# Kernel tuning notes

Hardware: AMD Instinct MI355X
Metric: run time of the kernel (lower is better)

Reference implementation:

```python
import jax, jax.numpy as jnp
import numpy as np

N_NODES = 50000
N_EDGES = 800000
N_GRAPHS = 512


def gcn_conv(x, W, b, src, dst, n_nodes):
    # Standard PyG GCNConv: linear transform, add self-loops, D^-1/2 (A+I) D^-1/2 aggregation.
    x = x @ W  # [N, out]
    loop = jnp.arange(n_nodes, dtype=src.dtype)
    s = jnp.concatenate([src, loop])  # [E+N]
    d = jnp.concatenate([dst, loop])
    deg = jax.ops.segment_sum(jnp.ones_like(d, dtype=x.dtype), d, num_segments=n_nodes)
    dinv = jnp.where(deg > 0, jax.lax.rsqrt(jnp.maximum(deg, 1e-12)), 0.0)
    norm = dinv[s] * dinv[d]  # [E+N]
    msg = x[s] * norm[:, None]  # gather + scale
    out = jax.ops.segment_sum(msg, d, num_segments=n_nodes)  # scatter-add
    return out + b


def setup_inputs() -> dict:
    key = jax.random.key(0)
    ks = jax.random.split(key, 10)
    x = jax.random.normal(ks[0], (N_NODES, 128), dtype=jnp.float32)
    edge_index = jax.random.randint(ks[1], (2, N_EDGES), 0, N_NODES, dtype=jnp.int64)
    batch = jnp.sort(jax.random.randint(ks[2], (N_NODES,), 0, N_GRAPHS, dtype=jnp.int64))
    y = jax.random.randint(ks[3], (N_GRAPHS,), 0, 4, dtype=jnp.int64)
    W1 = jax.random.normal(ks[4], (128, 64), dtype=jnp.float32) * (1.0 / np.sqrt(128))
    b1 = jnp.zeros((64,), dtype=jnp.float32)
    W2 = jax.random.normal(ks[5], (64, 64), dtype=jnp.float32) * (1.0 / np.sqrt(64))
    b2 = jnp.zeros((64,), dtype=jnp.float32)
    Wfc = jax.random.normal(ks[6], (64, 4), dtype=jnp.float32) * (1.0 / np.sqrt(64))
    bfc = jnp.zeros((4,), dtype=jnp.float32)
    return {"x": x, "edge_index": edge_index, "batch": batch, "y": y,
            "W1": W1, "b1": b1, "W2": W2, "b2": b2, "Wfc": Wfc, "bfc": bfc}


def reference(x, edge_index, batch, y, W1, b1, W2, b2, Wfc, bfc):
    src, dst = edge_index[0], edge_index[1]
    h = jax.nn.relu(gcn_conv(x, W1, b1, src, dst, N_NODES))
    h = jax.nn.relu(gcn_conv(h, W2, b2, src, dst, N_NODES))
    # global mean pool over graph ids
    sums = jax.ops.segment_sum(h, batch, num_segments=N_GRAPHS)  # [G, out]
    cnts = jax.ops.segment_sum(jnp.ones((h.shape[0],), h.dtype), batch, num_segments=N_GRAPHS)
    pooled = sums / jnp.maximum(cnts, 1.0)[:, None]
    logits = pooled @ Wfc + bfc
    logp = jax.nn.log_softmax(logits, axis=1)
    return (logp, y)
```

## Files before the change

kernel.cpp:

```cpp
#include <hip/hip_runtime.h>
#include <hip/hip_fp16.h>
#include <math.h>

#define N_NODES 50000
#define N_EDGES 800000
#define N_GRAPHS 512
#define NBKT 196
#define SENT N_NODES
#define EPB 2048
#define NSEG 391
#define CAP_C 48
#define NBLK_B2 392
#define CAP_SH 8192
#define NBLK_GM 782
#define PREP_GRID (NBLK_B2 + NBLK_GM)
#define N_GROUPS 6272
#define NBLK_G 1568

typedef float v2f __attribute__((ext_vector_type(2)));
typedef float f32x4 __attribute__((ext_vector_type(4)));
typedef short s16x8 __attribute__((ext_vector_type(8)));

#define OFF_DINV    0u
#define OFF_GGRP    200704u
#define OFF_CNTM    250880u
#define OFF_TMP     557568u
#define OFF_SORTED  15271680u
#define OFF_XS8_1   28116736u
#define OFF_XS8_2   31316992u
#define OFF_H2      34517248u

__device__ __forceinline__ unsigned short f2bf(float f) {
    unsigned int u = __float_as_uint(f);
    u += 0x7FFFu + ((u >> 16) & 1u);
    return (unsigned short)(u >> 16);
}

__global__ __launch_bounds__(256) void binA(const int* __restrict__ src, const int* __restrict__ dst,
                                            int* __restrict__ cntmat, unsigned int* __restrict__ tmp,
                                            unsigned int* __restrict__ x1, unsigned int* __restrict__ x2,
                                            float* __restrict__ dinv) {
    __shared__ int cnt[256];
    int t = threadIdx.x;
    cnt[t] = 0;
    if (blockIdx.x == 0) {
        if (t < 16) x1[N_NODES * 16 + t] = 0;
        else if (t < 32) x2[N_NODES * 16 + (t - 16)] = 0;
        else if (t >= 64 && t < 240) dinv[N_NODES + (t - 64)] = 0.0f;
    }
    __syncthreads();
    int e0 = blockIdx.x * EPB;
#pragma unroll
    for (int i = 0; i < 8; ++i) {
        int e = e0 + i * 256 + t;
        if (e < N_EDGES) {
            int s = src[e], d = dst[e];
            int b = d >> 8;
            int p = atomicAdd(&cnt[b], 1);
            tmp[(b * NSEG + blockIdx.x) * CAP_C + p] =
                (unsigned int)s | ((unsigned int)(d & 255) << 17);
        }
    }
    __syncthreads();
    if (t < NBKT) cntmat[blockIdx.x * NBKT + t] = cnt[t];
}

__global__ __launch_bounds__(256) void prep(const unsigned int* __restrict__ tmp,
                                            const int* __restrict__ cntmat,
                                            int* __restrict__ sorted, int2* __restrict__ ggrp,
                                            float* __restrict__ dinv,
                                            const float* __restrict__ X, const float* __restrict__ W1,
                                            unsigned int* __restrict__ xs8) {
    __shared__ __align__(16) char pool[35072];
    int t = threadIdx.x;

    if (blockIdx.x < NBLK_B2) {
        int* cnt  = (int*)pool;
        int* lbs  = (int*)(pool + 512);
        int* cur  = (int*)(pool + 1024);
        int* gK   = (int*)(pool + 1536);
        int* gpre = (int*)(pool + 1600);
        int* ldsS = (int*)(pool + 1792);
        int b2 = blockIdx.x, bkt = b2 >> 1, half = b2 & 1;
        if (t < 128) cnt[t] = 0;
        __syncthreads();
        for (int seg = t; seg < NSEG; seg += 256) {
            int c = cntmat[seg * NBKT + bkt];
            const unsigned int* tp = tmp + (bkt * NSEG + seg) * CAP_C;
            for (int e = 0; e < c; ++e) {
                int d = (int)(tp[e] >> 17);
                if ((d >> 7) == half) atomicAdd(&cnt[d & 127], 1);
            }
        }
        __syncthreads();
        int node = 0, deg = 0, K = 0, KP = 0, lb = 0, myreal = 0;
        if (t < 128) {
            node = bkt * 256 + half * 128 + t;
            myreal = node < N_NODES;
            deg = cnt[t];
            int count = myreal ? deg + 1 : 0;
            int mx = count;
            mx = max(mx, __shfl_xor(mx, 1));
            mx = max(mx, __shfl_xor(mx, 2));
            mx = max(mx, __shfl_xor(mx, 4));
            K = (mx + 3) & ~3;
            KP = K + 4;
            if ((t & 7) == 0) gK[t >> 3] = KP;
        }
        __syncthreads();
        if (t == 0) {
            int s = 0;
#pragma unroll
            for (int g = 0; g < 16; ++g) { gpre[g] = s; s += gK[g]; }
            gpre[16] = s;
        }
        __syncthreads();
        if (t < 128) {
            lb = 8 * gpre[t >> 3] + (t & 7);
            lbs[t] = lb;
            cur[t] = myreal ? 1 : 0;
            if (myreal) {
                dinv[node] = rsqrtf(1.0f + (float)deg);
                ldsS[lb] = node;
            }
            if ((t & 7) == 0)
                ggrp[b2 * 16 + (t >> 3)] = make_int2(b2 * CAP_SH + 8 * gpre[t >> 3], K);
        }
        __syncthreads();
        for (int seg = t; seg < NSEG; seg += 256) {
            int c = cntmat[seg * NBKT + bkt];
            const unsigned int* tp = tmp + (bkt * NSEG + seg) * CAP_C;
            for (int e = 0; e < c; ++e) {
                unsigned int pk = tp[e];
                int d = (int)(pk >> 17);
                if ((d >> 7) == half) {
                    int loc = d & 127;
                    int j = atomicAdd(&cur[loc], 1);
                    ldsS[lbs[loc] + j * 8] = (int)(pk & 0x1FFFFu);
                }
            }
        }
        __syncthreads();
        if (t < 128)
            for (int j = cur[t]; j < KP; ++j) ldsS[lb + j * 8] = SENT;
        __syncthreads();
        int ptot = 8 * gpre[16];
        int4* dst4 = (int4*)(sorted + b2 * CAP_SH);
        const int4* src4 = (const int4*)ldsS;
        for (int p = t; p < (ptot >> 2); p += 256) dst4[p] = src4[p];
    } else {
        short* W1T = (short*)pool;
        float* sD  = (float*)(pool + 17664);
        int gb = blockIdx.x - NBLK_B2;
        int row0 = gb * 64;
        for (int i = t; i < 8192; i += 256) {
            int k = i >> 6, c = i & 63;
            W1T[c * 138 + k] = (short)f2bf(W1[i]);
        }
        __syncthreads();
        int w = t >> 6, lane = t & 63;
        int arow = lane & 15, kg = lane >> 4;
        int r = row0 + w * 16 + arow;
        const float* xp = X + r * 128 + kg * 8;
        bool vr = (r < N_NODES);
        const short* wb = &W1T[arow * 138 + kg * 8];
        f32x4 ac0 = {0.f, 0.f, 0.f, 0.f}, ac1 = ac0, ac2 = ac0, ac3 = ac0;
#pragma unroll
        for (int kk = 0; kk < 4; ++kk) {
            float4 xa, xb;
            if (vr) { xa = *(const float4*)(xp); xb = *(const float4*)(xp + 4); }
            else    { xa = make_float4(0.f, 0.f, 0.f, 0.f); xb = xa; }
            xp += 32;
            s16x8 af;
            af[0] = (short)f2bf(xa.x); af[1] = (short)f2bf(xa.y);
            af[2] = (short)f2bf(xa.z); af[3] = (short)f2bf(xa.w);
            af[4] = (short)f2bf(xb.x); af[5] = (short)f2bf(xb.y);
            af[6] = (short)f2bf(xb.z); af[7] = (short)f2bf(xb.w);
            const short* wk = wb + kk * 32;
            s16x8 bf0 = *(const s16x8*)(wk);
            s16x8 bf1 = *(const s16x8*)(wk + 16 * 138);
            s16x8 bf2 = *(const s16x8*)(wk + 32 * 138);
            s16x8 bf3 = *(const s16x8*)(wk + 48 * 138);
            asm volatile(
                "s_nop 1\n\t"
                "v_mfma_f32_16x16x32_bf16 %0, %4, %5, %0\n\t"
                "v_mfma_f32_16x16x32_bf16 %1, %4, %6, %1\n\t"
                "v_mfma_f32_16x16x32_bf16 %2, %4, %7, %2\n\t"
                "v_mfma_f32_16x16x32_bf16 %3, %4, %8, %3"
                : "+v"(ac0), "+v"(ac1), "+v"(ac2), "+v"(ac3)
                : "v"(af), "v"(bf0), "v"(bf1), "v"(bf2), "v"(bf3));
        }
        asm volatile("s_nop 7\n\ts_nop 7");
        int dr = w * 16 + kg * 4;
#pragma unroll
        for (int reg = 0; reg < 4; ++reg) {
            sD[(dr + reg) * 68 + arow]      = ac0[reg];
            sD[(dr + reg) * 68 + 16 + arow] = ac1[reg];
            sD[(dr + reg) * 68 + 32 + arow] = ac2[reg];
            sD[(dr + reg) * 68 + 48 + arow] = ac3[reg];
        }
        __syncthreads();
        for (int i = t; i < 1024; i += 256) {
            int lr = i >> 4, q = i & 15;
            int nd = row0 + lr;
            if (nd < N_NODES) {
                float4 v = *(const float4*)&sD[lr * 68 + q * 4];
                unsigned int pk = 0;
                pk = __builtin_amdgcn_cvt_pk_fp8_f32(v.x, v.y, pk, false);
                pk = __builtin_amdgcn_cvt_pk_fp8_f32(v.z, v.w, pk, true);
                xs8[nd * 16 + q] = pk;
            }
        }
    }
}

#define ADD_ROW(rv) { \
    v2f f0 = __builtin_amdgcn_cvt_pk_f32_fp8((rv).x, false); \
    v2f f1 = __builtin_amdgcn_cvt_pk_f32_fp8((rv).x, true); \
    v2f f2 = __builtin_amdgcn_cvt_pk_f32_fp8((rv).y, false); \
    v2f f3 = __builtin_amdgcn_cvt_pk_f32_fp8((rv).y, true); \
    a0 += f0.x; a1 += f0.y; a2 += f1.x; a3 += f1.y; \
    a4 += f2.x; a5 += f2.y; a6 += f3.x; a7 += f3.y; }

#define FMA_ROW(rv, ds) { \
    v2f f0 = __builtin_amdgcn_cvt_pk_f32_fp8((rv).x, false); \
    v2f f1 = __builtin_amdgcn_cvt_pk_f32_fp8((rv).x, true); \
    v2f f2 = __builtin_amdgcn_cvt_pk_f32_fp8((rv).y, false); \
    v2f f3 = __builtin_amdgcn_cvt_pk_f32_fp8((rv).y, true); \
    a0 += f0.x * (ds); a1 += f0.y * (ds); a2 += f1.x * (ds); a3 += f1.y * (ds); \
    a4 += f2.x * (ds); a5 += f2.y * (ds); a6 += f3.x * (ds); a7 += f3.y * (ds); }

__global__ __launch_bounds__(256) void gather_fuse(const unsigned char* __restrict__ xs8,
                                                   const int2* __restrict__ ggrp,
                                                   const int* __restrict__ sorted,
                                                   const float* __restrict__ dinv,
                                                   const float* __restrict__ bias,
                                                   const float* __restrict__ W2,
                                                   unsigned int* __restrict__ xs8o) {
    __shared__ float sW2[64 * 64];
    __shared__ float sH[32][68];
    {
        const float4* ws = (const float4*)W2;
        float4* wd = (float4*)sW2;
        for (int i = threadIdx.x; i < 1024; i += 256) wd[i] = ws[i];
    }
    int wvl = threadIdx.x >> 6;
    int grp = blockIdx.x * 4 + wvl;

    int lane = threadIdx.x & 63;
    int sub = lane >> 3, frag = lane & 7;
    int node = grp * 8 + sub;
    int2 gi = ggrp[grp];
    int K = gi.y;
    const int* sp = sorted + gi.x + sub;
    const uint2* xr = (const uint2*)xs8 + frag;
    float a0 = 0, a1 = 0, a2 = 0, a3 = 0, a4 = 0, a5 = 0, a6 = 0, a7 = 0;
    int i0 = sp[0], i1 = sp[8], i2 = sp[16], i3 = sp[24];
    for (int k = 0; k < K; k += 4) {
        uint2 r0 = xr[i0 * 8];
        uint2 r1 = xr[i1 * 8];
        uint2 r2 = xr[i2 * 8];
        uint2 r3 = xr[i3 * 8];
        float s0 = dinv[i0], s1 = dinv[i1], s2 = dinv[i2], s3 = dinv[i3];
        const int* np = sp + (k + 4) * 8;
        i0 = np[0]; i1 = np[8]; i2 = np[16]; i3 = np[24];
        FMA_ROW(r0, s0); FMA_ROW(r1, s1); FMA_ROW(r2, s2); FMA_ROW(r3, s3);
    }
    {
        float dv = dinv[node];
        float4 bA = *(const float4*)(bias + frag * 8);
        float4 bB = *(const float4*)(bias + frag * 8 + 4);
        float4 w0, w1;
        w0.x = fmaxf(a0 * dv + bA.x, 0.0f); w0.y = fmaxf(a1 * dv + bA.y, 0.0f);
        w0.z = fmaxf(a2 * dv + bA.z, 0.0f); w0.w = fmaxf(a3 * dv + bA.w, 0.0f);
        w1.x = fmaxf(a4 * dv + bB.x, 0.0f); w1.y = fmaxf(a5 * dv + bB.y, 0.0f);
        w1.z = fmaxf(a6 * dv + bB.z, 0.0f); w1.w = fmaxf(a7 * dv + bB.w, 0.0f);
        *(float4*)&sH[wvl * 8 + sub][frag * 8] = w0;
        *(float4*)&sH[wvl * 8 + sub][frag * 8 + 4] = w1;
    }
    __syncthreads();
    int r = threadIdx.x >> 3;
    int cg = (threadIdx.x & 7) * 8;
    float b0 = 0, b1 = 0, b2 = 0, b3 = 0, b4 = 0, b5 = 0, b6 = 0, b7 = 0;
#pragma unroll 8
    for (int k = 0; k < 64; ++k) {
        float hv = sH[r][k];
        float4 wa = *(const float4*)&sW2[k * 64 + cg];
        float4 wbv = *(const float4*)&sW2[k * 64 + cg + 4];
        b0 += hv * wa.x; b1 += hv * wa.y; b2 += hv * wa.z; b3 += hv * wa.w;
        b4 += hv * wbv.x; b5 += hv * wbv.y; b6 += hv * wbv.z; b7 += hv * wbv.w;
    }
    int node2 = blockIdx.x * 32 + r;
    if (node2 < N_NODES) {
        float s = dinv[node2];
        unsigned int p0 = 0, p1 = 0;
        p0 = __builtin_amdgcn_cvt_pk_fp8_f32(b0 * s, b1 * s, p0, false);
        p0 = __builtin_amdgcn_cvt_pk_fp8_f32(b2 * s, b3 * s, p0, true);
        p1 = __builtin_amdgcn_cvt_pk_fp8_f32(b4 * s, b5 * s, p1, false);
        p1 = __builtin_amdgcn_cvt_pk_fp8_f32(b6 * s, b7 * s, p1, true);
        *(uint2*)(xs8o + node2 * 16 + (cg >> 2)) = make_uint2(p0, p1);
    }
}

__global__ __launch_bounds__(256) void gather_h2(const unsigned char* __restrict__ xs8,
                                                 const int2* __restrict__ ggrp,
                                                 const int* __restrict__ sorted,
                                                 const float* __restrict__ dinv,
                                                 const float* __restrict__ bias,
                                                 __half* __restrict__ h2) {
    int grp = blockIdx.x * 4 + (threadIdx.x >> 6);
    int lane = threadIdx.x & 63;
    int sub = lane >> 3, frag = lane & 7;
    int node = grp * 8 + sub;
    int2 gi = ggrp[grp];
    int K = gi.y;
    const int* sp = sorted + gi.x + sub;
    const uint2* xr = (const uint2*)xs8 + frag;
    float a0 = 0, a1 = 0, a2 = 0, a3 = 0, a4 = 0, a5 = 0, a6 = 0, a7 = 0;
    int i0 = sp[0], i1 = sp[8], i2 = sp[16], i3 = sp[24];
    for (int k = 0; k < K; k += 4) {
        uint2 r0 = xr[i0 * 8];
        uint2 r1 = xr[i1 * 8];
        uint2 r2 = xr[i2 * 8];
        uint2 r3 = xr[i3 * 8];
        const int* np = sp + (k + 4) * 8;
        i0 = np[0]; i1 = np[8]; i2 = np[16]; i3 = np[24];
        ADD_ROW(r0); ADD_ROW(r1); ADD_ROW(r2); ADD_ROW(r3);
    }
    if (node < N_NODES) {
        float dv = dinv[node];
        float4 bA = *(const float4*)(bias + frag * 8);
        float4 bB = *(const float4*)(bias + frag * 8 + 4);
        float v0 = fmaxf(a0 * dv + bA.x, 0.0f), v1 = fmaxf(a1 * dv + bA.y, 0.0f);
        float v2 = fmaxf(a2 * dv + bA.z, 0.0f), v3 = fmaxf(a3 * dv + bA.w, 0.0f);
        float v4 = fmaxf(a4 * dv + bB.x, 0.0f), v5 = fmaxf(a5 * dv + bB.y, 0.0f);
        float v6 = fmaxf(a6 * dv + bB.z, 0.0f), v7 = fmaxf(a7 * dv + bB.w, 0.0f);
        __half2 p0 = __floats2half2_rn(v0, v1), p1 = __floats2half2_rn(v2, v3);
        __half2 p2 = __floats2half2_rn(v4, v5), p3 = __floats2half2_rn(v6, v7);
        uint4 pk;
        pk.x = *(unsigned int*)&p0; pk.y = *(unsigned int*)&p1;
        pk.z = *(unsigned int*)&p2; pk.w = *(unsigned int*)&p3;
        *(uint4*)(h2 + node * 64 + frag * 8) = pk;
    }
}

__device__ __forceinline__ int lower_bound(const int* __restrict__ a, int n, int v) {
    int lo = 0, hi = n;
    while (lo < hi) { int m = (lo + hi) >> 1; if (a[m] < v) lo = m + 1; else hi = m; }
    return lo;
}

__global__ __launch_bounds__(256) void pool_head(const __half* __restrict__ h2,
                                                 const int* __restrict__ batch,
                                                 const float* __restrict__ Wfc, const float* __restrict__ bfc,
                                                 const int* __restrict__ y, float* __restrict__ out) {
    __shared__ int s_beg, s_end;
    __shared__ float sh[4][64];
    __shared__ float pl[64];
    __shared__ float lg[4];
    int g = blockIdx.x;
    int t = threadIdx.x;
    if (t == 0) s_beg = lower_bound(batch, N_NODES, g);
    if (t == 1) s_end = lower_bound(batch, N_NODES, g + 1);
    __syncthreads();
    int beg = s_beg, end = s_end;
    int f = t & 63, seg = t >> 6;
    float s = 0.0f;
    for (int r = beg + seg; r < end; r += 4) s += __half2float(h2[r * 64 + f]);
    sh[seg][f] = s;
    __syncthreads();
    if (t < 64) {
        float p = sh[0][t] + sh[1][t] + sh[2][t] + sh[3][t];
        pl[t] = p / fmaxf((float)(end - beg), 1.0f);
    }
    __syncthreads();
    if (t < 4) {
        float l = bfc[t];
#pragma unroll
        for (int k = 0; k < 64; ++k) l += pl[k] * Wfc[k * 4 + t];
        lg[t] = l;
    }
    __syncthreads();
    if (t == 0) {
        float l0 = lg[0], l1 = lg[1], l2 = lg[2], l3 = lg[3];
        float m = fmaxf(fmaxf(l0, l1), fmaxf(l2, l3));
        float ss = expf(l0 - m) + expf(l1 - m) + expf(l2 - m) + expf(l3 - m);
        float lse = m + logf(ss);
        out[g * 4 + 0] = l0 - lse;
        out[g * 4 + 1] = l1 - lse;
        out[g * 4 + 2] = l2 - lse;
        out[g * 4 + 3] = l3 - lse;
        out[N_GRAPHS * 4 + g] = (float)y[g];
    }
}

extern "C" void kernel_launch(void* const* d_in, const int* in_sizes, int n_in,
                              void* d_out, int out_size, void* d_ws, size_t ws_size,
                              hipStream_t stream) {
    const float* x     = (const float*)d_in[0];
    const int*   ei    = (const int*)d_in[1];
    const int*   batch = (const int*)d_in[2];
    const int*   y     = (const int*)d_in[3];
    const float* W1    = (const float*)d_in[4];
    const float* b1    = (const float*)d_in[5];
    const float* W2    = (const float*)d_in[6];
    const float* b2    = (const float*)d_in[7];
    const float* Wfc   = (const float*)d_in[8];
    const float* bfc   = (const float*)d_in[9];
    float* out = (float*)d_out;

    const int* src = ei;
    const int* dst = ei + N_EDGES;

    char* wsb = (char*)d_ws;
    float*        dinv   = (float*)(wsb + OFF_DINV);
    int2*         ggrp   = (int2*)(wsb + OFF_GGRP);
    int*          cntmat = (int*)(wsb + OFF_CNTM);
    unsigned int* tmp    = (unsigned int*)(wsb + OFF_TMP);
    int*          sorted = (int*)(wsb + OFF_SORTED);
    unsigned int* xs8_1  = (unsigned int*)(wsb + OFF_XS8_1);
    unsigned int* xs8_2  = (unsigned int*)(wsb + OFF_XS8_2);
    __half*       h2     = (__half*)(wsb + OFF_H2);

    binA<<<NSEG, 256, 0, stream>>>(src, dst, cntmat, tmp, xs8_1, xs8_2, dinv);
    prep<<<PREP_GRID, 256, 0, stream>>>(tmp, cntmat, sorted, ggrp, dinv, x, W1, xs8_1);
    gather_fuse<<<NBLK_G, 256, 0, stream>>>((const unsigned char*)xs8_1, ggrp, sorted,
                                            dinv, b1, W2, xs8_2);
    gather_h2<<<NBLK_G, 256, 0, stream>>>((const unsigned char*)xs8_2, ggrp, sorted,
                                          dinv, b2, h2);
    pool_head<<<N_GRAPHS, 256, 0, stream>>>(h2, batch, Wfc, bfc, y, out);
}
```

Measured before the change: 189.3 us.

## Flatten bucket scans, precompute graph bounds, move dinv scale into gather

The per-bucket edge bins are widened to 64 slots per segment, so prep can read each bucket as one flat coalesced sweep with a per-slot validity test instead of running a serial per-thread loop over each segment. binA now also computes per-graph node boundaries from the sorted batch vector, which lets pool_head skip two binary searches per block. The W1 LDS row stride changes from 138 to 136 shorts. In the second layer, the dinv source scaling moves out of the stored fp8 features and into the gather, which loads dinv per neighbour. This trades extra scanned slots, a larger workspace and extra per-edge loads for better memory parallelism, and storing h1 unscaled in fp8 may change precision.

```diff
diff --git a/kernel.cpp b/kernel.cpp
--- a/kernel.cpp
+++ b/kernel.cpp
@@ -9,13 +9,14 @@
 #define SENT N_NODES
 #define EPB 2048
 #define NSEG 391
-#define CAP_C 48
+#define CAP_C 64
 #define NBLK_B2 392
 #define CAP_SH 8192
 #define NBLK_GM 782
 #define PREP_GRID (NBLK_B2 + NBLK_GM)
 #define N_GROUPS 6272
 #define NBLK_G 1568
+#define SLOTS_B (NSEG * CAP_C)
 
 typedef float v2f __attribute__((ext_vector_type(2)));
 typedef float f32x4 __attribute__((ext_vector_type(4)));
@@ -24,11 +25,12 @@
 #define OFF_DINV    0u
 #define OFF_GGRP    200704u
 #define OFF_CNTM    250880u
-#define OFF_TMP     557568u
-#define OFF_SORTED  15271680u
-#define OFF_XS8_1   28116736u
-#define OFF_XS8_2   31316992u
-#define OFF_H2      34517248u
+#define OFF_GB      557568u
+#define OFF_TMP     559872u
+#define OFF_SORTED  20178688u
+#define OFF_XS8_1   33023744u
+#define OFF_XS8_2   36224000u
+#define OFF_H2      39424256u
 
 __device__ __forceinline__ unsigned short f2bf(float f) {
     unsigned int u = __float_as_uint(f);
@@ -37,16 +39,31 @@
 }
 
 __global__ __launch_bounds__(256) void binA(const int* __restrict__ src, const int* __restrict__ dst,
+                                            const int* __restrict__ batch,
                                             int* __restrict__ cntmat, unsigned int* __restrict__ tmp,
                                             unsigned int* __restrict__ x1, unsigned int* __restrict__ x2,
-                                            float* __restrict__ dinv) {
+                                            float* __restrict__ dinv, int* __restrict__ gbound) {
     __shared__ int cnt[256];
     int t = threadIdx.x;
     cnt[t] = 0;
     if (blockIdx.x == 0) {
         if (t < 16) x1[N_NODES * 16 + t] = 0;
         else if (t < 32) x2[N_NODES * 16 + (t - 16)] = 0;
-        else if (t >= 64 && t < 240) dinv[N_NODES + (t - 64)] = 0.0f;
+        else if (t == 32) dinv[SENT] = 0.0f;
+    }
+    if (blockIdx.x < 25) {
+        int i0 = blockIdx.x * 2048;
+#pragma unroll
+        for (int it = 0; it < 8; ++it) {
+            int i = i0 + it * 256 + t;
+            if (i < N_NODES) {
+                int b0 = batch[i];
+                int b1 = (i + 1 < N_NODES) ? batch[i + 1] : N_GRAPHS;
+                for (int g = b0 + 1; g <= b1; ++g) gbound[g] = i + 1;
+                if (i == 0)
+                    for (int g = 0; g <= b0; ++g) gbound[g] = 0;
+            }
+        }
     }
     __syncthreads();
     int e0 = blockIdx.x * EPB;
@@ -57,7 +74,7 @@
             int s = src[e], d = dst[e];
             int b = d >> 8;
             int p = atomicAdd(&cnt[b], 1);
-            tmp[(b * NSEG + blockIdx.x) * CAP_C + p] =
+            tmp[((b * NSEG + blockIdx.x) << 6) + p] =
                 (unsigned int)s | ((unsigned int)(d & 255) << 17);
         }
     }
@@ -71,7 +88,7 @@
                                             float* __restrict__ dinv,
                                             const float* __restrict__ X, const float* __restrict__ W1,
                                             unsigned int* __restrict__ xs8) {
-    __shared__ __align__(16) char pool[35072];
+    __shared__ __align__(16) char pool[36352];
     int t = threadIdx.x;
 
     if (blockIdx.x < NBLK_B2) {
@@ -80,15 +97,17 @@
         int* cur  = (int*)(pool + 1024);
         int* gK   = (int*)(pool + 1536);
         int* gpre = (int*)(pool + 1600);
-        int* ldsS = (int*)(pool + 1792);
+        int* cseg = (int*)(pool + 1792);
+        int* ldsS = (int*)(pool + 3584);
         int b2 = blockIdx.x, bkt = b2 >> 1, half = b2 & 1;
         if (t < 128) cnt[t] = 0;
-        __syncthreads();
-        for (int seg = t; seg < NSEG; seg += 256) {
-            int c = cntmat[seg * NBKT + bkt];
-            const unsigned int* tp = tmp + (bkt * NSEG + seg) * CAP_C;
-            for (int e = 0; e < c; ++e) {
-                int d = (int)(tp[e] >> 17);
+        for (int i = t; i < NSEG; i += 256) cseg[i] = cntmat[i * NBKT + bkt];
+        __syncthreads();
+        const unsigned int* tp = tmp + bkt * SLOTS_B;
+        for (int i = t; i < SLOTS_B; i += 256) {
+            unsigned int pk = tp[i];
+            if ((i & 63) < cseg[i >> 6]) {
+                int d = (int)(pk >> 17);
                 if ((d >> 7) == half) atomicAdd(&cnt[d & 127], 1);
             }
         }
@@ -127,11 +146,9 @@
                 ggrp[b2 * 16 + (t >> 3)] = make_int2(b2 * CAP_SH + 8 * gpre[t >> 3], K);
         }
         __syncthreads();
-        for (int seg = t; seg < NSEG; seg += 256) {
-            int c = cntmat[seg * NBKT + bkt];
-            const unsigned int* tp = tmp + (bkt * NSEG + seg) * CAP_C;
-            for (int e = 0; e < c; ++e) {
-                unsigned int pk = tp[e];
+        for (int i = t; i < SLOTS_B; i += 256) {
+            unsigned int pk = tp[i];
+            if ((i & 63) < cseg[i >> 6]) {
                 int d = (int)(pk >> 17);
                 if ((d >> 7) == half) {
                     int loc = d & 127;
@@ -150,12 +167,12 @@
         for (int p = t; p < (ptot >> 2); p += 256) dst4[p] = src4[p];
     } else {
         short* W1T = (short*)pool;
-        float* sD  = (float*)(pool + 17664);
+        float* sD  = (float*)(pool + 17408);
         int gb = blockIdx.x - NBLK_B2;
         int row0 = gb * 64;
         for (int i = t; i < 8192; i += 256) {
             int k = i >> 6, c = i & 63;
-            W1T[c * 138 + k] = (short)f2bf(W1[i]);
+            W1T[c * 136 + k] = (short)f2bf(W1[i]);
         }
         __syncthreads();
         int w = t >> 6, lane = t & 63;
@@ -163,7 +180,7 @@
         int r = row0 + w * 16 + arow;
         const float* xp = X + r * 128 + kg * 8;
         bool vr = (r < N_NODES);
-        const short* wb = &W1T[arow * 138 + kg * 8];
+        const short* wb = &W1T[arow * 136 + kg * 8];
         f32x4 ac0 = {0.f, 0.f, 0.f, 0.f}, ac1 = ac0, ac2 = ac0, ac3 = ac0;
 #pragma unroll
         for (int kk = 0; kk < 4; ++kk) {
@@ -178,9 +195,9 @@
             af[6] = (short)f2bf(xb.z); af[7] = (short)f2bf(xb.w);
             const short* wk = wb + kk * 32;
             s16x8 bf0 = *(const s16x8*)(wk);
-            s16x8 bf1 = *(const s16x8*)(wk + 16 * 138);
-            s16x8 bf2 = *(const s16x8*)(wk + 32 * 138);
-            s16x8 bf3 = *(const s16x8*)(wk + 48 * 138);
+            s16x8 bf1 = *(const s16x8*)(wk + 16 * 136);
+            s16x8 bf2 = *(const s16x8*)(wk + 32 * 136);
+            s16x8 bf3 = *(const s16x8*)(wk + 48 * 136);
             asm volatile(
                 "s_nop 1\n\t"
                 "v_mfma_f32_16x16x32_bf16 %0, %4, %5, %0\n\t"
@@ -213,14 +230,6 @@
         }
     }
 }
-
-#define ADD_ROW(rv) { \
-    v2f f0 = __builtin_amdgcn_cvt_pk_f32_fp8((rv).x, false); \
-    v2f f1 = __builtin_amdgcn_cvt_pk_f32_fp8((rv).x, true); \
-    v2f f2 = __builtin_amdgcn_cvt_pk_f32_fp8((rv).y, false); \
-    v2f f3 = __builtin_amdgcn_cvt_pk_f32_fp8((rv).y, true); \
-    a0 += f0.x; a1 += f0.y; a2 += f1.x; a3 += f1.y; \
-    a4 += f2.x; a5 += f2.y; a6 += f3.x; a7 += f3.y; }
 
 #define FMA_ROW(rv, ds) { \
     v2f f0 = __builtin_amdgcn_cvt_pk_f32_fp8((rv).x, false); \
@@ -292,12 +301,11 @@
     }
     int node2 = blockIdx.x * 32 + r;
     if (node2 < N_NODES) {
-        float s = dinv[node2];
         unsigned int p0 = 0, p1 = 0;
-        p0 = __builtin_amdgcn_cvt_pk_fp8_f32(b0 * s, b1 * s, p0, false);
-        p0 = __builtin_amdgcn_cvt_pk_fp8_f32(b2 * s, b3 * s, p0, true);
-        p1 = __builtin_amdgcn_cvt_pk_fp8_f32(b4 * s, b5 * s, p1, false);
-        p1 = __builtin_amdgcn_cvt_pk_fp8_f32(b6 * s, b7 * s, p1, true);
+        p0 = __builtin_amdgcn_cvt_pk_fp8_f32(b0, b1, p0, false);
+        p0 = __builtin_amdgcn_cvt_pk_fp8_f32(b2, b3, p0, true);
+        p1 = __builtin_amdgcn_cvt_pk_fp8_f32(b4, b5, p1, false);
+        p1 = __builtin_amdgcn_cvt_pk_fp8_f32(b6, b7, p1, true);
         *(uint2*)(xs8o + node2 * 16 + (cg >> 2)) = make_uint2(p0, p1);
     }
 }
@@ -323,9 +331,10 @@
         uint2 r1 = xr[i1 * 8];
         uint2 r2 = xr[i2 * 8];
         uint2 r3 = xr[i3 * 8];
+        float s0 = dinv[i0], s1 = dinv[i1], s2 = dinv[i2], s3 = dinv[i3];
         const int* np = sp + (k + 4) * 8;
         i0 = np[0]; i1 = np[8]; i2 = np[16]; i3 = np[24];
-        ADD_ROW(r0); ADD_ROW(r1); ADD_ROW(r2); ADD_ROW(r3);
+        FMA_ROW(r0, s0); FMA_ROW(r1, s1); FMA_ROW(r2, s2); FMA_ROW(r3, s3);
     }
     if (node < N_NODES) {
         float dv = dinv[node];
@@ -344,26 +353,16 @@
     }
 }
 
-__device__ __forceinline__ int lower_bound(const int* __restrict__ a, int n, int v) {
-    int lo = 0, hi = n;
-    while (lo < hi) { int m = (lo + hi) >> 1; if (a[m] < v) lo = m + 1; else hi = m; }
-    return lo;
-}
-
 __global__ __launch_bounds__(256) void pool_head(const __half* __restrict__ h2,
-                                                 const int* __restrict__ batch,
+                                                 const int* __restrict__ gbound,
                                                  const float* __restrict__ Wfc, const float* __restrict__ bfc,
                                                  const int* __restrict__ y, float* __restrict__ out) {
-    __shared__ int s_beg, s_end;
     __shared__ float sh[4][64];
     __shared__ float pl[64];
     __shared__ float lg[4];
     int g = blockIdx.x;
     int t = threadIdx.x;
-    if (t == 0) s_beg = lower_bound(batch, N_NODES, g);
-    if (t == 1) s_end = lower_bound(batch, N_NODES, g + 1);
-    __syncthreads();
-    int beg = s_beg, end = s_end;
+    int beg = gbound[g], end = gbound[g + 1];
     int f = t & 63, seg = t >> 6;
     float s = 0.0f;
     for (int r = beg + seg; r < end; r += 4) s += __half2float(h2[r * 64 + f]);
@@ -416,17 +415,18 @@
     float*        dinv   = (float*)(wsb + OFF_DINV);
     int2*         ggrp   = (int2*)(wsb + OFF_GGRP);
     int*          cntmat = (int*)(wsb + OFF_CNTM);
+    int*          gbound = (int*)(wsb + OFF_GB);
     unsigned int* tmp    = (unsigned int*)(wsb + OFF_TMP);
     int*          sorted = (int*)(wsb + OFF_SORTED);
     unsigned int* xs8_1  = (unsigned int*)(wsb + OFF_XS8_1);
     unsigned int* xs8_2  = (unsigned int*)(wsb + OFF_XS8_2);
     __half*       h2     = (__half*)(wsb + OFF_H2);
 
-    binA<<<NSEG, 256, 0, stream>>>(src, dst, cntmat, tmp, xs8_1, xs8_2, dinv);
+    binA<<<NSEG, 256, 0, stream>>>(src, dst, batch, cntmat, tmp, xs8_1, xs8_2, dinv, gbound);
     prep<<<PREP_GRID, 256, 0, stream>>>(tmp, cntmat, sorted, ggrp, dinv, x, W1, xs8_1);
     gather_fuse<<<NBLK_G, 256, 0, stream>>>((const unsigned char*)xs8_1, ggrp, sorted,
                                             dinv, b1, W2, xs8_2);
     gather_h2<<<NBLK_G, 256, 0, stream>>>((const unsigned char*)xs8_2, ggrp, sorted,
                                           dinv, b2, h2);
-    pool_head<<<N_GRAPHS, 256, 0, stream>>>(h2, batch, Wfc, bfc, y, out);
-}
+    pool_head<<<N_GRAPHS, 256, 0, stream>>>(h2, gbound, Wfc, bfc, y, out);
+}
```

Measured after the change: 216.3 us. +14.3%, slower.
